# Performance work log

Measured on AMD Instinct MI355X. Metric: run time of the kernel, lower is better.

Reference implementation:

```python
import jax, jax.numpy as jnp
import numpy as np
import math

C = 8  # sparsity factor c from __init__


def setup_inputs() -> dict:
    key = jax.random.key(0)
    kq, kk, kv, ki = jax.random.split(key, 4)
    B, Q, KV, D = 4, 2048, 2048, 512
    U = int(Q * math.log(KV))  # 15615 sampled keys, matches torch _sampler
    q = jax.random.normal(kq, (B, Q, D), dtype=jnp.float32)
    k = jax.random.normal(kk, (B, KV, D), dtype=jnp.float32)
    v = jax.random.normal(kv, (B, KV, D), dtype=jnp.float32)
    sample_idx = jax.random.randint(ki, (B, U), 0, KV)  # per-batch random key sample
    return {"q": q, "k": k, "v": v, "sample_idx": sample_idx}


def reference(q, k, v, sample_idx):
    B, Q, D = q.shape
    KV = k.shape[1]
    u = int(C * math.log(Q))  # number of selected queries (== 60 here)

    # _sampler: gather sampled keys per batch -> (B, U, D)
    k_bar = jnp.take_along_axis(k, sample_idx[:, :, None], axis=1)

    # sparsity measure M = max_j s_bar - mean_j s_bar, s_bar: (B, Q, U)
    s_bar = jnp.einsum('bqd,bud->bqu', q, k_bar)
    M = s_bar.max(axis=2) - s_bar.mean(axis=2)  # (B, Q)

    # top-u queries per batch
    _, top_idx = jax.lax.top_k(M, u)  # (B, u)
    q_bar = jnp.take_along_axis(q, top_idx[:, :, None], axis=1)  # (B, u, D)

    # small dense attention over full keys; NOTE: original scales by sqrt(kv_len)
    attn = jnp.einsum('bud,bkd->buk', q_bar, k) / jnp.sqrt(jnp.asarray(KV, q.dtype))
    attn = jax.nn.softmax(attn, axis=-1)
    s1 = jnp.einsum('buk,bkd->bud', attn, v)  # (B, u, D)

    # fill all positions with mean of v, then scatter attention outputs
    s = jnp.broadcast_to(v.mean(axis=1, keepdims=True), q.shape)  # (B, Q, D)
    bidx = jnp.arange(B)[:, None]
    s = s.at[bidx, top_idx].set(s1)
    return s
```

## Files before the change

kernel.cpp:

```cpp
#include <hip/hip_runtime.h>
#include <math.h>

#define BATCH 4
#define QN    2048
#define KVN   2048
#define DN    512
#define U_TOT 15615
#define NSEL  60
#define NSLOT 32
#define S1KS  32

typedef __attribute__((ext_vector_type(8))) short bf16x8;
typedef __attribute__((ext_vector_type(4))) float f32x4;

__device__ __forceinline__ unsigned short f2bf(float f) {
  unsigned u = __float_as_uint(f);
  unsigned r = (u + 0x7fffu + ((u >> 16) & 1u)) >> 16;
  return (unsigned short)r;
}
__device__ __forceinline__ float bf2f(unsigned short h) {
  return __uint_as_float(((unsigned)h) << 16);
}
__device__ __forceinline__ void gld16(const void* g, void* l) {
  __builtin_amdgcn_global_load_lds(
      (const __attribute__((address_space(1))) unsigned int*)g,
      (__attribute__((address_space(3))) unsigned int*)l, 16, 0, 0);
}

__global__ __launch_bounds__(256) void split_kernel(
    const float* __restrict__ q, const float* __restrict__ k,
    unsigned short* __restrict__ qhi, unsigned short* __restrict__ qlo,
    unsigned short* __restrict__ khi, unsigned short* __restrict__ klo)
{
  const int half = blockIdx.x >> 12;
  const int i = (blockIdx.x & 4095) * 256 + threadIdx.x;
  const float* in = half ? k : q;
  unsigned short* hi = half ? khi : qhi;
  unsigned short* lo = half ? klo : qlo;
  float4 f = reinterpret_cast<const float4*>(in)[i];
  ushort4 h, l;
  h.x = f2bf(f.x); l.x = f2bf(f.x - bf2f(h.x));
  h.y = f2bf(f.y); l.y = f2bf(f.y - bf2f(h.y));
  h.z = f2bf(f.z); l.z = f2bf(f.z - bf2f(h.z));
  h.w = f2bf(f.w); l.w = f2bf(f.w - bf2f(h.w));
  reinterpret_cast<ushort4*>(hi)[i] = h;
  reinterpret_cast<ushort4*>(lo)[i] = l;
}

__global__ __launch_bounds__(1024) void count_kernel(
    const int* __restrict__ sidx, float* __restrict__ cnt)
{
  __shared__ int h[KVN];
  const int b = blockIdx.x, t = threadIdx.x;
  for (int i = t; i < KVN; i += 1024) h[i] = 0;
  __syncthreads();
  for (int i = t; i < U_TOT; i += 1024) atomicAdd(&h[sidx[b * U_TOT + i]], 1);
  __syncthreads();
  for (int i = t; i < KVN; i += 1024) cnt[b * KVN + i] = (float)h[i];
}

#define BAR() asm volatile("s_barrier" ::: "memory")

#define PHASE_MFMA(P) \
  __builtin_amdgcn_s_setprio(1); \
  _Pragma("unroll") \
  for (int n = 0; n < 4; ++n) { \
    acc[2*(P)][n]   = __builtin_amdgcn_mfma_f32_16x16x32_bf16(a0h, bh_[n], acc[2*(P)][n], 0, 0, 0); \
    acc[2*(P)][n]   = __builtin_amdgcn_mfma_f32_16x16x32_bf16(a0h, bl_[n], acc[2*(P)][n], 0, 0, 0); \
    acc[2*(P)][n]   = __builtin_amdgcn_mfma_f32_16x16x32_bf16(a0l, bh_[n], acc[2*(P)][n], 0, 0, 0); \
    acc[2*(P)+1][n] = __builtin_amdgcn_mfma_f32_16x16x32_bf16(a1h, bh_[n], acc[2*(P)+1][n], 0, 0, 0); \
    acc[2*(P)+1][n] = __builtin_amdgcn_mfma_f32_16x16x32_bf16(a1h, bl_[n], acc[2*(P)+1][n], 0, 0, 0); \
    acc[2*(P)+1][n] = __builtin_amdgcn_mfma_f32_16x16x32_bf16(a1l, bh_[n], acc[2*(P)+1][n], 0, 0, 0); \
  } \
  __builtin_amdgcn_s_setprio(0);

#define LOAD_A(P, CB) \
  a0h = *reinterpret_cast<const bf16x8*>(&Ah[CB][(4*(P)+wr)*512 + fr8]); \
  a0l = *reinterpret_cast<const bf16x8*>(&Al[CB][(4*(P)+wr)*512 + fr8]); \
  a1h = *reinterpret_cast<const bf16x8*>(&Ah[CB][(4*(P)+2+wr)*512 + fr8]); \
  a1l = *reinterpret_cast<const bf16x8*>(&Al[CB][(4*(P)+2+wr)*512 + fr8]);

#define LOAD_B(CB) \
  _Pragma("unroll") \
  for (int n = 0; n < 4; ++n) { \
    bh_[n] = *reinterpret_cast<const bf16x8*>(&Bh[CB][wc*2048 + n*512 + fr8]); \
    bl_[n] = *reinterpret_cast<const bf16x8*>(&Bl[CB][wc*2048 + n*512 + fr8]); \
  }

#define KSTEP_MAIN(CB, NB) { \
  gld16(kh0, &Bh[NB][t*8]); gld16(kh1, &Bh[NB][4096 + t*8]); \
  gld16(kl0, &Bl[NB][t*8]); gld16(kl1, &Bl[NB][4096 + t*8]); \
  gld16(qh0, &Ah[NB][t*8]); gld16(ql0, &Al[NB][t*8]); \
  gld16(qh1, &Ah[NB][4096 + t*8]); gld16(ql1, &Al[NB][4096 + t*8]); \
  kh0 += 32; kh1 += 32; kl0 += 32; kl1 += 32; \
  qh0 += 32; qh1 += 32; ql0 += 32; ql1 += 32; \
  { \
    bf16x8 bh_[4], bl_[4], a0h, a0l, a1h, a1l; \
    LOAD_B(CB) \
    LOAD_A(0, CB) \
    PHASE_MFMA(0) \
    LOAD_A(1, CB) \
    PHASE_MFMA(1) \
    LOAD_A(2, CB) \
    PHASE_MFMA(2) \
    LOAD_A(3, CB) \
    PHASE_MFMA(3) \
  } \
  asm volatile("s_waitcnt vmcnt(0)" ::: "memory"); \
  BAR(); \
}

#define KSTEP_LAST(CB) { \
  bf16x8 bh_[4], bl_[4], a0h, a0l, a1h, a1l; \
  LOAD_B(CB) \
  LOAD_A(0, CB) \
  PHASE_MFMA(0) \
  LOAD_A(1, CB) \
  PHASE_MFMA(1) \
  LOAD_A(2, CB) \
  PHASE_MFMA(2) \
  LOAD_A(3, CB) \
  PHASE_MFMA(3) \
}

__global__ __launch_bounds__(512, 2) void s_mfma_kernel(
    const unsigned short* __restrict__ qh, const unsigned short* __restrict__ ql,
    const unsigned short* __restrict__ kh, const unsigned short* __restrict__ kl,
    const float* __restrict__ cnt, float* __restrict__ Pmax, float* __restrict__ Psum)
{
  __shared__ __align__(16) unsigned short Ah[2][8192];
  __shared__ __align__(16) unsigned short Al[2][8192];
  __shared__ __align__(16) unsigned short Bh[2][8192];
  __shared__ __align__(16) unsigned short Bl[2][8192];
  __shared__ float cnt_s[256];

  const int t = threadIdx.x;
  const int w = t >> 6;
  const int L = t & 63;
  const int lm = L & 15;
  const int wr = w >> 2;
  const int wc = w & 3;

  const int bid = blockIdx.x;
  const int xcd = bid & 7;
  const int idx = bid >> 3;
  const int b   = xcd >> 1;
  const int ji  = (xcd & 1) * 4 + (idx >> 3);
  const int qi  = idx & 7;
  const int j0  = ji * 256;
  const int q0  = qi * 256;

  if (t < 256) cnt_s[t] = cnt[b * KVN + j0 + t];

  const int srow = t >> 2;
  const int schk = (t & 3) ^ ((t >> 3) & 3);
  const int perm = (L >> 4) ^ ((lm >> 1) & 3);
  const int fr8  = (4 * lm + perm) * 8;

  const size_t kof = ((size_t)(b * KVN) + j0 + srow) * DN + (size_t)(schk * 8);
  const size_t qof = ((size_t)(b * QN) + q0 + srow) * DN + (size_t)(schk * 8);
  const unsigned short* kh0 = kh + kof;
  const unsigned short* kh1 = kh0 + (size_t)128 * DN;
  const unsigned short* kl0 = kl + kof;
  const unsigned short* kl1 = kl0 + (size_t)128 * DN;
  const unsigned short* qh0 = qh + qof;
  const unsigned short* qh1 = qh0 + (size_t)128 * DN;
  const unsigned short* ql0 = ql + qof;
  const unsigned short* ql1 = ql0 + (size_t)128 * DN;

  f32x4 acc[8][4];
#pragma unroll
  for (int m = 0; m < 8; ++m)
#pragma unroll
    for (int n = 0; n < 4; ++n) {
      acc[m][n][0] = 0.f; acc[m][n][1] = 0.f;
      acc[m][n][2] = 0.f; acc[m][n][3] = 0.f;
    }

  gld16(kh0, &Bh[0][t*8]); gld16(kh1, &Bh[0][4096 + t*8]);
  gld16(kl0, &Bl[0][t*8]); gld16(kl1, &Bl[0][4096 + t*8]);
  gld16(qh0, &Ah[0][t*8]); gld16(ql0, &Al[0][t*8]);
  gld16(qh1, &Ah[0][4096 + t*8]); gld16(ql1, &Al[0][4096 + t*8]);
  kh0 += 32; kh1 += 32; kl0 += 32; kl1 += 32;
  qh0 += 32; qh1 += 32; ql0 += 32; ql1 += 32;
  asm volatile("s_waitcnt vmcnt(0) lgkmcnt(0)" ::: "memory");
  BAR();

#pragma unroll 1
  for (int it = 0; it < 7; ++it) {
    KSTEP_MAIN(0, 1)
    KSTEP_MAIN(1, 0)
  }
  KSTEP_MAIN(0, 1)
  KSTEP_LAST(1)

  const int slot = ji * 4 + wc;
  const size_t spi = (size_t)(slot * BATCH + b);
  const int rgrp = (L >> 4) * 4;
#pragma unroll
  for (int m = 0; m < 8; ++m) {
    float mx[4] = {-INFINITY, -INFINITY, -INFINITY, -INFINITY};
    float ws[4] = {0.f, 0.f, 0.f, 0.f};
#pragma unroll
    for (int n = 0; n < 4; ++n) {
      const float cw = cnt_s[wc * 64 + n * 16 + lm];
      const bool has = (cw > 0.f);
#pragma unroll
      for (int r = 0; r < 4; ++r) {
        const float v = acc[m][n][r];
        if (has) mx[r] = fmaxf(mx[r], v);
        ws[r] = fmaf(cw, v, ws[r]);
      }
    }
#pragma unroll
    for (int r = 0; r < 4; ++r) {
      float mval = mx[r], sval = ws[r];
#pragma unroll
      for (int o = 1; o < 16; o <<= 1) {
        mval = fmaxf(mval, __shfl_xor(mval, o));
        sval += __shfl_xor(sval, o);
      }
      if (lm == 0) {
        const int qrow = q0 + (2 * m + wr) * 16 + rgrp + r;
        Pmax[spi * QN + qrow] = mval;
        Psum[spi * QN + qrow] = sval;
      }
    }
  }
}

__global__ __launch_bounds__(256) void combine_kernel(
    const float* __restrict__ Pmax, const float* __restrict__ Psum, float* __restrict__ M)
{
  const int g = blockIdx.x * 256 + threadIdx.x;
  const int b = g >> 11;
  const int qq = g & (QN - 1);
  float m = -INFINITY, s = 0.f;
#pragma unroll 4
  for (int p = 0; p < NSLOT; ++p) {
    m = fmaxf(m, Pmax[((size_t)(p * BATCH + b)) * QN + qq]);
    s += Psum[((size_t)(p * BATCH + b)) * QN + qq];
  }
  M[g] = m - s * (1.0f / (float)U_TOT);
}

__global__ __launch_bounds__(256) void select_kernel(
    const float* __restrict__ M, int* __restrict__ topidx, int* __restrict__ rowslot)
{
  const int b = blockIdx.x;
  const int t = threadIdx.x;
  unsigned long long key[8];
#pragma unroll
  for (int s = 0; s < 8; ++s) {
    const int qq = s * 256 + t;
    unsigned u = __float_as_uint(M[b * QN + qq]);
    u = (u & 0x80000000u) ? ~u : (u | 0x80000000u);
    key[s] = ((unsigned long long)u << 32) | (unsigned)(QN - qq);
    rowslot[b * QN + qq] = -1;
  }

  __shared__ unsigned hist[256];
  __shared__ unsigned long long pref_s;
  __shared__ unsigned rank_s;
  __shared__ unsigned cnt_s;
  if (t == 0) { pref_s = 0ull; rank_s = NSEL; cnt_s = 0u; }
  __syncthreads();

  for (int level = 7; level >= 0; --level) {
    const int shift = level * 8;
    hist[t] = 0;
    __syncthreads();
    const unsigned long long pref = pref_s;
    const unsigned rank = rank_s;
#pragma unroll
    for (int s = 0; s < 8; ++s) {
      const bool match = (level == 7) || ((key[s] >> (shift + 8)) == pref);
      if (match) atomicAdd(&hist[(unsigned)((key[s] >> shift) & 255u)], 1u);
    }
    __syncthreads();
    if (t < 64) {
      const unsigned h0 = hist[4 * t], h1 = hist[4 * t + 1];
      const unsigned h2 = hist[4 * t + 2], h3 = hist[4 * t + 3];
      const unsigned loc = h0 + h1 + h2 + h3;
      unsigned run = loc;
#pragma unroll
      for (int o = 1; o < 64; o <<= 1) {
        const unsigned oth = (unsigned)__shfl_down((int)run, o);
        if (t + o < 64) run += oth;
      }
      const unsigned suf = run - loc;
      const unsigned c3 = suf, c2 = c3 + h3, c1 = c2 + h2, c0 = c1 + h1;
      int hit = -1; unsigned cgt = 0;
      if      (c3 < rank && rank <= c3 + h3) { hit = 4 * t + 3; cgt = c3; }
      else if (c2 < rank && rank <= c2 + h2) { hit = 4 * t + 2; cgt = c2; }
      else if (c1 < rank && rank <= c1 + h1) { hit = 4 * t + 1; cgt = c1; }
      else if (c0 < rank && rank <= c0 + h0) { hit = 4 * t + 0; cgt = c0; }
      if (hit >= 0) {
        pref_s = ((level == 7) ? 0ull : (pref_s << 8)) | (unsigned long long)(unsigned)hit;
        rank_s = rank - cgt;
      }
    }
    __syncthreads();
  }

  const unsigned long long T = pref_s;
#pragma unroll
  for (int s = 0; s < 8; ++s) {
    if (key[s] >= T) {
      const unsigned pos = atomicAdd(&cnt_s, 1u);
      const int qsel = QN - (int)(key[s] & 0xFFFFFFFFull);
      topidx[b * 64 + pos] = qsel;
      rowslot[b * QN + qsel] = (int)pos;
    }
  }
}

#define SBM 64
#define SBN 32
#define SBK 32
__global__ __launch_bounds__(256) void scores_kernel(
    const float* __restrict__ q, const int* __restrict__ topidx,
    const float* __restrict__ k, float* __restrict__ attn)
{
  __shared__ float a_s[SBK][SBM + 4];
  __shared__ float b_s[SBK][SBN + 4];
  __shared__ int tix_s[64];
  const int t  = threadIdx.x;
  const int tx = t & 7;
  const int ty = t >> 3;
  const int kv0 = blockIdx.x * SBN;
  const int b   = blockIdx.y;
  const float* kb = k + (size_t)b * KVN * DN;

  if (t < 64) tix_s[t] = (t < NSEL) ? topidx[b * 64 + t] : 0;
  __syncthreads();

  float acc[2][4];
#pragma unroll
  for (int i = 0; i < 2; ++i)
#pragma unroll
    for (int j = 0; j < 4; ++j) acc[i][j] = 0.f;

  const int c4 = (t & 7) * 4;
  const int r0 = t >> 3;
  const int srow0 = tix_s[r0];
  const int srow1 = tix_s[r0 + 32];

  for (int d0 = 0; d0 < DN; d0 += SBK) {
#pragma unroll
    for (int rr = 0; rr < 2; ++rr) {
      int row = r0 + rr * 32;
      int srow = rr ? srow1 : srow0;
      float4 av = *reinterpret_cast<const float4*>(q + ((size_t)(b * QN) + srow) * DN + d0 + c4);
      a_s[c4 + 0][row] = av.x; a_s[c4 + 1][row] = av.y;
      a_s[c4 + 2][row] = av.z; a_s[c4 + 3][row] = av.w;
    }
    {
      float4 bv = *reinterpret_cast<const float4*>(kb + (size_t)(kv0 + r0) * DN + d0 + c4);
      b_s[c4 + 0][r0] = bv.x; b_s[c4 + 1][r0] = bv.y;
      b_s[c4 + 2][r0] = bv.z; b_s[c4 + 3][r0] = bv.w;
    }
    __syncthreads();
#pragma unroll
    for (int kk = 0; kk < SBK; ++kk) {
      const float a0 = a_s[kk][ty * 2];
      const float a1 = a_s[kk][ty * 2 + 1];
      float4 bv = *reinterpret_cast<const float4*>(&b_s[kk][tx * 4]);
      float bf[4] = {bv.x, bv.y, bv.z, bv.w};
#pragma unroll
      for (int j = 0; j < 4; ++j) {
        acc[0][j] = fmaf(a0, bf[j], acc[0][j]);
        acc[1][j] = fmaf(a1, bf[j], acc[1][j]);
      }
    }
    __syncthreads();
  }

  const float sc = 0.022097086912079608f;
#pragma unroll
  for (int i = 0; i < 2; ++i) {
    int j = ty * 2 + i;
    if (j < NSEL) {
      float4 o = make_float4(__expf(acc[i][0] * sc), __expf(acc[i][1] * sc),
                             __expf(acc[i][2] * sc), __expf(acc[i][3] * sc));
      *reinterpret_cast<float4*>(attn + ((size_t)(b * NSEL + j)) * KVN + kv0 + tx * 4) = o;
    }
  }
}

__global__ __launch_bounds__(256) void s1_partial_kernel(
    const float* __restrict__ attn, const float* __restrict__ v,
    float* __restrict__ part, float* __restrict__ epart, float* __restrict__ vpart)
{
  __shared__ float a_s[64][61];
  const int t    = threadIdx.x;
  const int dv4  = t & 63;
  const int jg   = t >> 6;
  const int dh   = blockIdx.x;
  const int b    = blockIdx.y;
  const int ks   = blockIdx.z;
  const int kv0  = ks * 64;
  const int dbase = dh * 256 + dv4 * 4;

  for (int x = t; x < NSEL * 64; x += 256) {
    const int j = x >> 6, kk = x & 63;
    a_s[kk][j] = attn[((size_t)(b * NSEL + j)) * KVN + kv0 + kk];
  }
  __syncthreads();

  if (dh == 0 && t < NSEL) {
    float es = 0.f;
    for (int kk = 0; kk < 64; ++kk) es += a_s[kk][t];
    epart[(ks * BATCH + b) * 64 + t] = es;
  }

  f32x4 acc[15];
#pragma unroll
  for (int i = 0; i < 15; ++i) { acc[i][0] = 0.f; acc[i][1] = 0.f; acc[i][2] = 0.f; acc[i][3] = 0.f; }
  f32x4 vsum; vsum[0] = 0.f; vsum[1] = 0.f; vsum[2] = 0.f; vsum[3] = 0.f;

  const float* vb = v + ((size_t)b * KVN + kv0) * DN + dbase;
#pragma unroll 4
  for (int kk = 0; kk < 64; ++kk) {
    const f32x4 vv = *reinterpret_cast<const f32x4*>(vb + (size_t)kk * DN);
    if (jg == 0) { vsum[0] += vv[0]; vsum[1] += vv[1]; vsum[2] += vv[2]; vsum[3] += vv[3]; }
#pragma unroll
    for (int jj = 0; jj < 15; ++jj) {
      const float a = a_s[kk][jg * 15 + jj];
      acc[jj][0] = fmaf(a, vv[0], acc[jj][0]);
      acc[jj][1] = fmaf(a, vv[1], acc[jj][1]);
      acc[jj][2] = fmaf(a, vv[2], acc[jj][2]);
      acc[jj][3] = fmaf(a, vv[3], acc[jj][3]);
    }
  }

#pragma unroll
  for (int jj = 0; jj < 15; ++jj) {
    const int j = jg * 15 + jj;
    *reinterpret_cast<f32x4*>(
        part + ((size_t)((ks * BATCH + b) * NSEL) + j) * DN + dbase) = acc[jj];
  }
  if (jg == 0)
    *reinterpret_cast<f32x4*>(vpart + ((size_t)(ks * BATCH + b)) * DN + dbase) = vsum;
}

__global__ void vmean_combine_kernel(const float* __restrict__ vpart,
                                     const float* __restrict__ epart,
                                     float* __restrict__ vmean, float* __restrict__ einv)
{
  int idx = blockIdx.x * 256 + threadIdx.x;
  if (idx < BATCH * DN) {
    int b = idx / DN, d = idx % DN;
    float s = 0.f;
    for (int c = 0; c < S1KS; ++c) s += vpart[(size_t)(c * BATCH + b) * DN + d];
    vmean[idx] = s * (1.0f / (float)KVN);
  } else if (idx < BATCH * DN + BATCH * 64) {
    int i2 = idx - BATCH * DN;
    int b = i2 >> 6, s = i2 & 63;
    float es = 0.f;
    for (int c = 0; c < S1KS; ++c) es += epart[(c * BATCH + b) * 64 + s];
    einv[i2] = 1.f / es;
  }
}

__global__ __launch_bounds__(256) void out_kernel(
    const float* __restrict__ part, const float* __restrict__ einv,
    const float* __restrict__ vmean, const int* __restrict__ rowslot,
    float* __restrict__ out)
{
  const int gid = blockIdx.x * 256 + threadIdx.x;
  const int d4 = gid & 127;
  const int qq = (gid >> 7) & (QN - 1);
  const int b  = gid >> 18;
  const int slot = rowslot[b * QN + qq];
  f32x4 o;
  if (slot >= 0) {
    o[0] = 0.f; o[1] = 0.f; o[2] = 0.f; o[3] = 0.f;
    for (int ks = 0; ks < S1KS; ++ks) {
      const f32x4 p = reinterpret_cast<const f32x4*>(part)[
          ((size_t)((ks * BATCH + b) * NSEL) + slot) * (DN / 4) + d4];
      o[0] += p[0]; o[1] += p[1]; o[2] += p[2]; o[3] += p[3];
    }
    const float inv = einv[b * 64 + slot];
    o[0] *= inv; o[1] *= inv; o[2] *= inv; o[3] *= inv;
  } else {
    o = reinterpret_cast<const f32x4*>(vmean)[b * (DN / 4) + d4];
  }
  reinterpret_cast<f32x4*>(out)[gid] = o;
}

extern "C" void kernel_launch(void* const* d_in, const int* in_sizes, int n_in,
                              void* d_out, int out_size, void* d_ws, size_t ws_size,
                              hipStream_t stream) {
  const float* q    = (const float*)d_in[0];
  const float* k    = (const float*)d_in[1];
  const float* v    = (const float*)d_in[2];
  const int*   sidx = (const int*)d_in[3];
  float* out = (float*)d_out;
  char*  W   = (char*)d_ws;

  const size_t NEL = (size_t)BATCH * QN * DN;
  unsigned short* qh = (unsigned short*)W;
  unsigned short* ql = qh + NEL;
  unsigned short* kh = ql + NEL;
  unsigned short* kl = kh + NEL;

  char* W2 = W + 37748736;
  float* cnt     = (float*)W2;
  float* Pmax    = (float*)(W2 + 32768);
  float* Psum    = (float*)(W2 + 32768 + 1048576);
  float* Mbuf    = (float*)(W2 + 32768 + 2097152);
  int*   topidx  = (int*)(W2 + 32768 + 2097152 + 32768);
  int*   rowslot = (int*)(W2 + 32768 + 2097152 + 32768 + 4096);

  float* attn  = (float*)W;
  float* part  = (float*)(W + 2097152);
  float* vpart = (float*)(W + 33554432);
  float* vmean = (float*)(W + 34078720);
  float* epart = (float*)(W + 34209792);
  float* einv  = (float*)(W + 34242560);

  split_kernel<<<dim3(8192), 256, 0, stream>>>(q, k, qh, ql, kh, kl);
  count_kernel<<<dim3(BATCH), 1024, 0, stream>>>(sidx, cnt);
  s_mfma_kernel<<<dim3(256), 512, 0, stream>>>(qh, ql, kh, kl, cnt, Pmax, Psum);
  combine_kernel<<<dim3(BATCH * QN / 256), 256, 0, stream>>>(Pmax, Psum, Mbuf);
  select_kernel<<<dim3(BATCH), 256, 0, stream>>>(Mbuf, topidx, rowslot);
  scores_kernel<<<dim3(KVN / SBN, BATCH), 256, 0, stream>>>(q, topidx, k, attn);
  s1_partial_kernel<<<dim3(2, BATCH, S1KS), 256, 0, stream>>>(attn, v, part, epart, vpart);
  vmean_combine_kernel<<<dim3(9), 256, 0, stream>>>(vpart, epart, vmean, einv);
  out_kernel<<<dim3(4096), 256, 0, stream>>>(part, einv, vmean, rowslot, out);
}
```

Baseline: 219.7 us.

## Halve key tile, drop LDS double buffering, double grid for s_mfma and s1

The sampled-score MFMA kernel now uses 128-key tiles instead of 256, giving 512 blocks instead of 256. Shared memory is single-buffered so more blocks fit per CU (launch bounds 4), at the cost of losing load/compute overlap and adding an extra barrier per k-step. The s1 partial kernel is split over 64 KV chunks of 32 instead of 32 of 64. Partial-max/sum slots and workspace offsets are doubled to match. The aim is better CU occupancy and parallelism for the 256 CUs, traded against more partial results to combine and less data reuse per block.

New measurement: 223.2 us. Within noise of the previous version (+1.6%).

```diff
diff --git a/kernel.cpp b/kernel.cpp
--- a/kernel.cpp
+++ b/kernel.cpp
@@ -7,8 +7,8 @@
 #define DN    512
 #define U_TOT 15615
 #define NSEL  60
-#define NSLOT 32
-#define S1KS  32
+#define NSLOT 64
+#define S1KS  64
 
 typedef __attribute__((ext_vector_type(8))) short bf16x8;
 typedef __attribute__((ext_vector_type(4))) float f32x4;
@@ -64,7 +64,7 @@
 #define PHASE_MFMA(P) \
   __builtin_amdgcn_s_setprio(1); \
   _Pragma("unroll") \
-  for (int n = 0; n < 4; ++n) { \
+  for (int n = 0; n < 2; ++n) { \
     acc[2*(P)][n]   = __builtin_amdgcn_mfma_f32_16x16x32_bf16(a0h, bh_[n], acc[2*(P)][n], 0, 0, 0); \
     acc[2*(P)][n]   = __builtin_amdgcn_mfma_f32_16x16x32_bf16(a0h, bl_[n], acc[2*(P)][n], 0, 0, 0); \
     acc[2*(P)][n]   = __builtin_amdgcn_mfma_f32_16x16x32_bf16(a0l, bh_[n], acc[2*(P)][n], 0, 0, 0); \
@@ -74,65 +74,49 @@
   } \
   __builtin_amdgcn_s_setprio(0);
 
-#define LOAD_A(P, CB) \
-  a0h = *reinterpret_cast<const bf16x8*>(&Ah[CB][(4*(P)+wr)*512 + fr8]); \
-  a0l = *reinterpret_cast<const bf16x8*>(&Al[CB][(4*(P)+wr)*512 + fr8]); \
-  a1h = *reinterpret_cast<const bf16x8*>(&Ah[CB][(4*(P)+2+wr)*512 + fr8]); \
-  a1l = *reinterpret_cast<const bf16x8*>(&Al[CB][(4*(P)+2+wr)*512 + fr8]);
-
-#define LOAD_B(CB) \
+#define LOAD_A(P) \
+  a0h = *reinterpret_cast<const bf16x8*>(&Ah[(4*(P)+wr)*512 + fr8]); \
+  a0l = *reinterpret_cast<const bf16x8*>(&Al[(4*(P)+wr)*512 + fr8]); \
+  a1h = *reinterpret_cast<const bf16x8*>(&Ah[(4*(P)+2+wr)*512 + fr8]); \
+  a1l = *reinterpret_cast<const bf16x8*>(&Al[(4*(P)+2+wr)*512 + fr8]);
+
+#define LOAD_B() \
   _Pragma("unroll") \
-  for (int n = 0; n < 4; ++n) { \
-    bh_[n] = *reinterpret_cast<const bf16x8*>(&Bh[CB][wc*2048 + n*512 + fr8]); \
-    bl_[n] = *reinterpret_cast<const bf16x8*>(&Bl[CB][wc*2048 + n*512 + fr8]); \
-  }
-
-#define KSTEP_MAIN(CB, NB) { \
-  gld16(kh0, &Bh[NB][t*8]); gld16(kh1, &Bh[NB][4096 + t*8]); \
-  gld16(kl0, &Bl[NB][t*8]); gld16(kl1, &Bl[NB][4096 + t*8]); \
-  gld16(qh0, &Ah[NB][t*8]); gld16(ql0, &Al[NB][t*8]); \
-  gld16(qh1, &Ah[NB][4096 + t*8]); gld16(ql1, &Al[NB][4096 + t*8]); \
-  kh0 += 32; kh1 += 32; kl0 += 32; kl1 += 32; \
-  qh0 += 32; qh1 += 32; ql0 += 32; ql1 += 32; \
-  { \
-    bf16x8 bh_[4], bl_[4], a0h, a0l, a1h, a1l; \
-    LOAD_B(CB) \
-    LOAD_A(0, CB) \
-    PHASE_MFMA(0) \
-    LOAD_A(1, CB) \
-    PHASE_MFMA(1) \
-    LOAD_A(2, CB) \
-    PHASE_MFMA(2) \
-    LOAD_A(3, CB) \
-    PHASE_MFMA(3) \
-  } \
-  asm volatile("s_waitcnt vmcnt(0)" ::: "memory"); \
-  BAR(); \
-}
-
-#define KSTEP_LAST(CB) { \
-  bf16x8 bh_[4], bl_[4], a0h, a0l, a1h, a1l; \
-  LOAD_B(CB) \
-  LOAD_A(0, CB) \
+  for (int n = 0; n < 2; ++n) { \
+    bh_[n] = *reinterpret_cast<const bf16x8*>(&Bh[(wc*2 + n)*512 + fr8]); \
+    bl_[n] = *reinterpret_cast<const bf16x8*>(&Bl[(wc*2 + n)*512 + fr8]); \
+  }
+
+#define KSTEP_COMPUTE() { \
+  bf16x8 bh_[2], bl_[2], a0h, a0l, a1h, a1l; \
+  LOAD_B() \
+  LOAD_A(0) \
   PHASE_MFMA(0) \
-  LOAD_A(1, CB) \
+  LOAD_A(1) \
   PHASE_MFMA(1) \
-  LOAD_A(2, CB) \
+  LOAD_A(2) \
   PHASE_MFMA(2) \
-  LOAD_A(3, CB) \
+  LOAD_A(3) \
   PHASE_MFMA(3) \
 }
 
-__global__ __launch_bounds__(512, 2) void s_mfma_kernel(
+#define STAGE() { \
+  gld16(qh0, &Ah[t*8]); gld16(qh1, &Ah[4096 + t*8]); \
+  gld16(ql0, &Al[t*8]); gld16(ql1, &Al[4096 + t*8]); \
+  gld16(kh0, &Bh[t*8]); gld16(kl0, &Bl[t*8]); \
+  qh0 += 32; qh1 += 32; ql0 += 32; ql1 += 32; kh0 += 32; kl0 += 32; \
+}
+
+__global__ __launch_bounds__(512, 4) void s_mfma_kernel(
     const unsigned short* __restrict__ qh, const unsigned short* __restrict__ ql,
     const unsigned short* __restrict__ kh, const unsigned short* __restrict__ kl,
     const float* __restrict__ cnt, float* __restrict__ Pmax, float* __restrict__ Psum)
 {
-  __shared__ __align__(16) unsigned short Ah[2][8192];
-  __shared__ __align__(16) unsigned short Al[2][8192];
-  __shared__ __align__(16) unsigned short Bh[2][8192];
-  __shared__ __align__(16) unsigned short Bl[2][8192];
-  __shared__ float cnt_s[256];
+  __shared__ __align__(16) unsigned short Ah[8192];
+  __shared__ __align__(16) unsigned short Al[8192];
+  __shared__ __align__(16) unsigned short Bh[4096];
+  __shared__ __align__(16) unsigned short Bl[4096];
+  __shared__ float cnt_s[128];
 
   const int t = threadIdx.x;
   const int w = t >> 6;
@@ -145,12 +129,12 @@
   const int xcd = bid & 7;
   const int idx = bid >> 3;
   const int b   = xcd >> 1;
-  const int ji  = (xcd & 1) * 4 + (idx >> 3);
+  const int ji  = (xcd & 1) * 8 + (idx >> 3);
   const int qi  = idx & 7;
-  const int j0  = ji * 256;
+  const int j0  = ji * 128;
   const int q0  = qi * 256;
 
-  if (t < 256) cnt_s[t] = cnt[b * KVN + j0 + t];
+  if (t < 128) cnt_s[t] = cnt[b * KVN + j0 + t];
 
   const int srow = t >> 2;
   const int schk = (t & 3) ^ ((t >> 3) & 3);
@@ -160,39 +144,34 @@
   const size_t kof = ((size_t)(b * KVN) + j0 + srow) * DN + (size_t)(schk * 8);
   const size_t qof = ((size_t)(b * QN) + q0 + srow) * DN + (size_t)(schk * 8);
   const unsigned short* kh0 = kh + kof;
-  const unsigned short* kh1 = kh0 + (size_t)128 * DN;
   const unsigned short* kl0 = kl + kof;
-  const unsigned short* kl1 = kl0 + (size_t)128 * DN;
   const unsigned short* qh0 = qh + qof;
   const unsigned short* qh1 = qh0 + (size_t)128 * DN;
   const unsigned short* ql0 = ql + qof;
   const unsigned short* ql1 = ql0 + (size_t)128 * DN;
 
-  f32x4 acc[8][4];
+  f32x4 acc[8][2];
 #pragma unroll
   for (int m = 0; m < 8; ++m)
 #pragma unroll
-    for (int n = 0; n < 4; ++n) {
+    for (int n = 0; n < 2; ++n) {
       acc[m][n][0] = 0.f; acc[m][n][1] = 0.f;
       acc[m][n][2] = 0.f; acc[m][n][3] = 0.f;
     }
 
-  gld16(kh0, &Bh[0][t*8]); gld16(kh1, &Bh[0][4096 + t*8]);
-  gld16(kl0, &Bl[0][t*8]); gld16(kl1, &Bl[0][4096 + t*8]);
-  gld16(qh0, &Ah[0][t*8]); gld16(ql0, &Al[0][t*8]);
-  gld16(qh1, &Ah[0][4096 + t*8]); gld16(ql1, &Al[0][4096 + t*8]);
-  kh0 += 32; kh1 += 32; kl0 += 32; kl1 += 32;
-  qh0 += 32; qh1 += 32; ql0 += 32; ql1 += 32;
+  STAGE();
   asm volatile("s_waitcnt vmcnt(0) lgkmcnt(0)" ::: "memory");
   BAR();
 
 #pragma unroll 1
-  for (int it = 0; it < 7; ++it) {
-    KSTEP_MAIN(0, 1)
-    KSTEP_MAIN(1, 0)
-  }
-  KSTEP_MAIN(0, 1)
-  KSTEP_LAST(1)
+  for (int it = 0; it < 15; ++it) {
+    KSTEP_COMPUTE();
+    BAR();
+    STAGE();
+    asm volatile("s_waitcnt vmcnt(0)" ::: "memory");
+    BAR();
+  }
+  KSTEP_COMPUTE();
 
   const int slot = ji * 4 + wc;
   const size_t spi = (size_t)(slot * BATCH + b);
@@ -202,8 +181,8 @@
     float mx[4] = {-INFINITY, -INFINITY, -INFINITY, -INFINITY};
     float ws[4] = {0.f, 0.f, 0.f, 0.f};
 #pragma unroll
-    for (int n = 0; n < 4; ++n) {
-      const float cw = cnt_s[wc * 64 + n * 16 + lm];
+    for (int n = 0; n < 2; ++n) {
+      const float cw = cnt_s[wc * 32 + n * 16 + lm];
       const bool has = (cw > 0.f);
 #pragma unroll
       for (int r = 0; r < 4; ++r) {
@@ -392,25 +371,25 @@
     const float* __restrict__ attn, const float* __restrict__ v,
     float* __restrict__ part, float* __restrict__ epart, float* __restrict__ vpart)
 {
-  __shared__ float a_s[64][61];
+  __shared__ float a_s[32][61];
   const int t    = threadIdx.x;
   const int dv4  = t & 63;
   const int jg   = t >> 6;
   const int dh   = blockIdx.x;
   const int b    = blockIdx.y;
   const int ks   = blockIdx.z;
-  const int kv0  = ks * 64;
+  const int kv0  = ks * 32;
   const int dbase = dh * 256 + dv4 * 4;
 
-  for (int x = t; x < NSEL * 64; x += 256) {
-    const int j = x >> 6, kk = x & 63;
+  for (int x = t; x < NSEL * 32; x += 256) {
+    const int j = x >> 5, kk = x & 31;
     a_s[kk][j] = attn[((size_t)(b * NSEL + j)) * KVN + kv0 + kk];
   }
   __syncthreads();
 
   if (dh == 0 && t < NSEL) {
     float es = 0.f;
-    for (int kk = 0; kk < 64; ++kk) es += a_s[kk][t];
+    for (int kk = 0; kk < 32; ++kk) es += a_s[kk][t];
     epart[(ks * BATCH + b) * 64 + t] = es;
   }
 
@@ -420,8 +399,8 @@
   f32x4 vsum; vsum[0] = 0.f; vsum[1] = 0.f; vsum[2] = 0.f; vsum[3] = 0.f;
 
   const float* vb = v + ((size_t)b * KVN + kv0) * DN + dbase;
-#pragma unroll 4
-  for (int kk = 0; kk < 64; ++kk) {
+#pragma unroll 8
+  for (int kk = 0; kk < 32; ++kk) {
     const f32x4 vv = *reinterpret_cast<const f32x4*>(vb + (size_t)kk * DN);
     if (jg == 0) { vsum[0] += vv[0]; vsum[1] += vv[1]; vsum[2] += vv[2]; vsum[3] += vv[3]; }
 #pragma unroll
@@ -508,21 +487,21 @@
   char* W2 = W + 37748736;
   float* cnt     = (float*)W2;
   float* Pmax    = (float*)(W2 + 32768);
-  float* Psum    = (float*)(W2 + 32768 + 1048576);
-  float* Mbuf    = (float*)(W2 + 32768 + 2097152);
-  int*   topidx  = (int*)(W2 + 32768 + 2097152 + 32768);
-  int*   rowslot = (int*)(W2 + 32768 + 2097152 + 32768 + 4096);
+  float* Psum    = (float*)(W2 + 32768 + 2097152);
+  float* Mbuf    = (float*)(W2 + 32768 + 4194304);
+  int*   topidx  = (int*)(W2 + 32768 + 4194304 + 32768);
+  int*   rowslot = (int*)(W2 + 32768 + 4194304 + 32768 + 4096);
 
   float* attn  = (float*)W;
   float* part  = (float*)(W + 2097152);
   float* vpart = (float*)(W + 33554432);
   float* vmean = (float*)(W + 34078720);
   float* epart = (float*)(W + 34209792);
-  float* einv  = (float*)(W + 34242560);
+  float* einv  = (float*)(W + 34275328);
 
   split_kernel<<<dim3(8192), 256, 0, stream>>>(q, k, qh, ql, kh, kl);
   count_kernel<<<dim3(BATCH), 1024, 0, stream>>>(sidx, cnt);
-  s_mfma_kernel<<<dim3(256), 512, 0, stream>>>(qh, ql, kh, kl, cnt, Pmax, Psum);
+  s_mfma_kernel<<<dim3(512), 512, 0, stream>>>(qh, ql, kh, kl, cnt, Pmax, Psum);
   combine_kernel<<<dim3(BATCH * QN / 256), 256, 0, stream>>>(Pmax, Psum, Mbuf);
   select_kernel<<<dim3(BATCH), 256, 0, stream>>>(Mbuf, topidx, rowslot);
   scores_kernel<<<dim3(KVN / SBN, BATCH), 256, 0, stream>>>(q, topidx, k, attn);
```
